# Kernel optimization log

Measured on AMD Instinct MI355X. Metric: run time of the kernel, lower is better.

## Reference

```python
import jax, jax.numpy as jnp
import numpy as np

N, K, D = 50000, 32, 128


def setup_inputs() -> dict:
    key = jax.random.key(0)
    k1, k2, k3, k4 = jax.random.split(key, 4)
    v_fea = jax.random.normal(k1, (N, D), dtype=jnp.float32)
    t_emb = jax.random.normal(k2, (N, D), dtype=jnp.float32)
    ef = jax.random.randint(k3, (N, K), 0, N, dtype=jnp.int64)
    # nn.Linear(2D, 2D, bias=False) weight, scaled like torch default init
    W = jax.random.normal(k4, (2 * D, 2 * D), dtype=jnp.float32) * (1.0 / np.sqrt(2 * D))
    return {"v_fea": v_fea, "t_emb": t_emb, "ef": ef, "W": W}


def reference(v_fea, t_emb, ef, W):
    # v: gathered neighbor features [N, K, D]
    v = v_fea[ef]
    # q: [N, 2D]; torch Linear applies x @ W.T
    q = jnp.concatenate([v_fea, t_emb], axis=-1)
    wq = q @ W.T                                   # [N, 2D]
    # k: [N, K, 2D]
    k = jnp.concatenate([v, t_emb[ef]], axis=-1)
    # per-edge score: bmm(k, wq[..., None]) -> [N, K]
    r = jnp.einsum("nkd,nd->nk", k, wq)
    r = jax.nn.softmax(r, axis=1)                  # softmax over neighbors
    # weighted sum over neighbors -> [N, D]
    ef_fea = jnp.einsum("nk,nkd->nd", r, v)
    return ef_fea
```

## Files before the change

kernel.cpp:

```cpp
#include <hip/hip_runtime.h>
#include <hip/hip_bf16.h>

#define D     128
#define TWO_D 256
#define KNB   32

typedef __attribute__((ext_vector_type(8))) short    s8;
typedef __attribute__((ext_vector_type(8))) _Float16 h8;
typedef __attribute__((ext_vector_type(4))) float    f4;

__device__ inline unsigned short f2h(float f) {
    return __builtin_bit_cast(unsigned short, (_Float16)f);
}
__device__ inline float h2f(unsigned short u) {
    return (float)__builtin_bit_cast(_Float16, u);
}

__global__ __launch_bounds__(256) void cast_kernel(
    const float* __restrict__ a, const float* __restrict__ b,
    unsigned short* __restrict__ oa, unsigned short* __restrict__ ob, int n4)
{
    int i = blockIdx.x * 256 + threadIdx.x;
    if (i >= n4) return;
    float4 x = ((const float4*)a)[i];
    float4 y = ((const float4*)b)[i];
    ushort4 px = make_ushort4(f2h(x.x), f2h(x.y), f2h(x.z), f2h(x.w));
    ushort4 py = make_ushort4(f2h(y.x), f2h(y.y), f2h(y.z), f2h(y.w));
    ((ushort4*)oa)[i] = px;
    ((ushort4*)ob)[i] = py;
}

#define BM 128
#define BN 128
#define BK 32
#define LDT 56

template<bool WQ_F32>
__global__ __launch_bounds__(256) void gemm_wq_mfma(
    const float* __restrict__ v_fea, const float* __restrict__ t_emb,
    const float* __restrict__ W, float* __restrict__ wq_f,
    unsigned short* __restrict__ wq_h, int M)
{
    __shared__ unsigned short As[BM][LDT];
    __shared__ unsigned short Bs[BN][LDT];

    const int tid  = threadIdx.x;
    const int w    = tid >> 6;
    const int lane = tid & 63;
    const int quad = lane >> 4;
    const int l16  = lane & 15;
    const int row0 = blockIdx.x * BM;
    const int i0   = blockIdx.y * BN;

    f4 acc[2][8] = {};

    const int srow = tid >> 1;
    const int skh  = (tid & 1) * 16;
    int ga = row0 + srow; if (ga >= M) ga = M - 1;

    for (int kt = 0; kt < TWO_D; kt += BK) {
        const float* srcA = (kt < D) ? v_fea : t_emb;
        const int kb = kt & (D - 1);
        const float* pa = srcA + (size_t)ga * D + kb + skh;
        const float* pb = W + (size_t)(i0 + srow) * TWO_D + kt + skh;
        float4 av0 = *(const float4*)(pa);
        float4 av1 = *(const float4*)(pa + 4);
        float4 av2 = *(const float4*)(pa + 8);
        float4 av3 = *(const float4*)(pa + 12);
        float4 bv0 = *(const float4*)(pb);
        float4 bv1 = *(const float4*)(pb + 4);
        float4 bv2 = *(const float4*)(pb + 8);
        float4 bv3 = *(const float4*)(pb + 12);

        __syncthreads();
        {
            s8 p0, p1;
            p0[0]=(short)f2h(av0.x); p0[1]=(short)f2h(av0.y); p0[2]=(short)f2h(av0.z); p0[3]=(short)f2h(av0.w);
            p0[4]=(short)f2h(av1.x); p0[5]=(short)f2h(av1.y); p0[6]=(short)f2h(av1.z); p0[7]=(short)f2h(av1.w);
            p1[0]=(short)f2h(av2.x); p1[1]=(short)f2h(av2.y); p1[2]=(short)f2h(av2.z); p1[3]=(short)f2h(av2.w);
            p1[4]=(short)f2h(av3.x); p1[5]=(short)f2h(av3.y); p1[6]=(short)f2h(av3.z); p1[7]=(short)f2h(av3.w);
            *(s8*)&As[srow][skh]     = p0;
            *(s8*)&As[srow][skh + 8] = p1;
            s8 q0, q1;
            q0[0]=(short)f2h(bv0.x); q0[1]=(short)f2h(bv0.y); q0[2]=(short)f2h(bv0.z); q0[3]=(short)f2h(bv0.w);
            q0[4]=(short)f2h(bv1.x); q0[5]=(short)f2h(bv1.y); q0[6]=(short)f2h(bv1.z); q0[7]=(short)f2h(bv1.w);
            q1[0]=(short)f2h(bv2.x); q1[1]=(short)f2h(bv2.y); q1[2]=(short)f2h(bv2.z); q1[3]=(short)f2h(bv2.w);
            q1[4]=(short)f2h(bv3.x); q1[5]=(short)f2h(bv3.y); q1[6]=(short)f2h(bv3.z); q1[7]=(short)f2h(bv3.w);
            *(s8*)&Bs[srow][skh]     = q0;
            *(s8*)&Bs[srow][skh + 8] = q1;
        }
        __syncthreads();

        s8 af0 = *(const s8*)&As[w * 32 + l16][quad * 8];
        s8 af1 = *(const s8*)&As[w * 32 + 16 + l16][quad * 8];
#pragma unroll
        for (int nt = 0; nt < 8; ++nt) {
            s8 bf = *(const s8*)&Bs[nt * 16 + l16][quad * 8];
            acc[0][nt] = __builtin_amdgcn_mfma_f32_16x16x32_f16(
                __builtin_bit_cast(h8, af0), __builtin_bit_cast(h8, bf), acc[0][nt], 0, 0, 0);
            acc[1][nt] = __builtin_amdgcn_mfma_f32_16x16x32_f16(
                __builtin_bit_cast(h8, af1), __builtin_bit_cast(h8, bf), acc[1][nt], 0, 0, 0);
        }
    }

#pragma unroll
    for (int mt = 0; mt < 2; ++mt) {
#pragma unroll
        for (int nt = 0; nt < 8; ++nt) {
#pragma unroll
            for (int r = 0; r < 4; ++r) {
                int grow = row0 + w * 32 + mt * 16 + quad * 4 + r;
                if (grow < M) {
                    int gcol = i0 + nt * 16 + l16;
                    if (WQ_F32) wq_f[(size_t)grow * TWO_D + gcol] = acc[mt][nt][r];
                    else        wq_h[(size_t)grow * TWO_D + gcol] = f2h(acc[mt][nt][r]);
                }
            }
        }
    }
}

template<bool WQ_F32>
__global__ __launch_bounds__(256) void attn_kernel(
    const unsigned short* __restrict__ vh, const unsigned short* __restrict__ th,
    const int* __restrict__ ef, const float* __restrict__ wq_f,
    const unsigned short* __restrict__ wq_h, float* __restrict__ outp, int M)
{
    __shared__ unsigned short v_cache[4][KNB][D];

    const int lane = threadIdx.x & 63;
    const int w    = threadIdx.x >> 6;
    const int n    = blockIdx.x * 4 + w;
    if (n >= M) return;

    const int l16  = lane & 15;
    const int gsel = (lane >> 4) & 1;
    const unsigned short* gsrc = (lane < 32) ? vh : th;

    float wv[8];
    if (WQ_F32) {
        const float* p = wq_f + (size_t)n * TWO_D + ((lane >> 5) << 7) + l16 * 8;
        float4 c0 = *(const float4*)p;
        float4 c1 = *(const float4*)(p + 4);
        wv[0]=c0.x; wv[1]=c0.y; wv[2]=c0.z; wv[3]=c0.w;
        wv[4]=c1.x; wv[5]=c1.y; wv[6]=c1.z; wv[7]=c1.w;
    } else {
        s8 h = *(const s8*)(wq_h + (size_t)n * TWO_D + ((lane >> 5) << 7) + l16 * 8);
#pragma unroll
        for (int j = 0; j < 8; ++j) wv[j] = h2f((unsigned short)h[j]);
    }

    int eidx = 0;
    if (lane < KNB) eidx = ef[n * KNB + lane];

    float myscore = -1e30f;
#pragma unroll
    for (int k = 0; k < KNB; k += 2) {
        int e = __shfl(eidx, k + gsel, 64);
        s8 x = *(const s8*)(gsrc + (size_t)e * D + l16 * 8);
        if (lane < 32) *(s8*)&v_cache[w][k + gsel][l16 * 8] = x;
        float p = 0.f;
#pragma unroll
        for (int j = 0; j < 8; ++j) p = fmaf(h2f((unsigned short)x[j]), wv[j], p);
#pragma unroll
        for (int off = 8; off > 0; off >>= 1) p += __shfl_xor(p, off, 64);
        p += __shfl_xor(p, 32, 64);
        float po = __shfl_xor(p, 16, 64);
        float s_even = gsel ? po : p;
        float s_odd  = gsel ? p  : po;
        if (lane == k)     myscore = s_even;
        if (lane == k + 1) myscore = s_odd;
    }

    float mx = myscore;
#pragma unroll
    for (int off = 16; off > 0; off >>= 1) mx = fmaxf(mx, __shfl_xor(mx, off, 64));
    float ex  = __expf(myscore - mx);
    float sum = ex;
#pragma unroll
    for (int off = 16; off > 0; off >>= 1) sum += __shfl_xor(sum, off, 64);
    float r = ex / sum;

    float2 o = make_float2(0.f, 0.f);
#pragma unroll
    for (int k = 0; k < KNB; ++k) {
        float rk = __shfl(r, k, 64);
        unsigned int pq = *(const unsigned int*)&v_cache[w][k][lane * 2];
        o.x = fmaf(rk, h2f((unsigned short)(pq & 0xFFFFu)), o.x);
        o.y = fmaf(rk, h2f((unsigned short)(pq >> 16)), o.y);
    }
    *(float2*)(outp + (size_t)n * D + lane * 2) = o;
}

extern "C" void kernel_launch(void* const* d_in, const int* in_sizes, int n_in,
                              void* d_out, int out_size, void* d_ws, size_t ws_size,
                              hipStream_t stream)
{
    const float* v_fea = (const float*)d_in[0];
    const float* t_emb = (const float*)d_in[1];
    const int*   ef    = (const int*)d_in[2];
    const float* W     = (const float*)d_in[3];
    float* outp = (float*)d_out;

    const int M = in_sizes[0] / D;
    const size_t gath = (size_t)M * D * 2;
    const size_t wq_f32_bytes = (size_t)M * TWO_D * 4;
    const bool wqf32 = ws_size >= wq_f32_bytes + 2 * gath;

    char* ws = (char*)d_ws;
    float*          wq_f = (float*)ws;
    unsigned short* wq_h = (unsigned short*)ws;
    const size_t wq_bytes = wqf32 ? wq_f32_bytes : (size_t)M * TWO_D * 2;
    unsigned short* vh = (unsigned short*)(ws + wq_bytes);
    unsigned short* th = (unsigned short*)(ws + wq_bytes + gath);

    const int n4 = M * D / 4;
    cast_kernel<<<(n4 + 255) / 256, 256, 0, stream>>>(v_fea, t_emb, vh, th, n4);

    dim3 gg((M + BM - 1) / BM, TWO_D / BN);
    if (wqf32) {
        gemm_wq_mfma<true><<<gg, 256, 0, stream>>>(v_fea, t_emb, W, wq_f, wq_h, M);
        attn_kernel<true><<<(M + 3) / 4, 256, 0, stream>>>(vh, th, ef, wq_f, wq_h, outp, M);
    } else {
        gemm_wq_mfma<false><<<gg, 256, 0, stream>>>(v_fea, t_emb, W, wq_f, wq_h, M);
        attn_kernel<false><<<(M + 3) / 4, 256, 0, stream>>>(vh, th, ef, wq_f, wq_h, outp, M);
    }
}
```

Before: 251.5 us.

## Use fp16 wq always, read pre-cast inputs in GEMM, batch gathers, use fdot2

The GEMM now loads the fp16 copies of v_fea/t_emb produced by the cast kernel instead of re-reading and converting fp32 inputs. wq is always stored in fp16, which halves its write and read traffic. The attention kernel issues all 16 gather loads up front to raise memory-level parallelism, and computes scores with packed fp16 dot2 instructions. The costs are more live registers (16 s8 vectors) and slightly lower score precision from the fp16 wq.

```diff
diff --git a/kernel.cpp b/kernel.cpp
--- a/kernel.cpp
+++ b/kernel.cpp
@@ -7,6 +7,7 @@
 
 typedef __attribute__((ext_vector_type(8))) short    s8;
 typedef __attribute__((ext_vector_type(8))) _Float16 h8;
+typedef __attribute__((ext_vector_type(2))) _Float16 h2v;
 typedef __attribute__((ext_vector_type(4))) float    f4;
 
 __device__ inline unsigned short f2h(float f) {
@@ -14,6 +15,22 @@
 }
 __device__ inline float h2f(unsigned short u) {
     return (float)__builtin_bit_cast(_Float16, u);
+}
+
+union v16u { s8 s; h2v h[4]; };
+
+__device__ inline float dot8(s8 x, s8 w, float acc) {
+#if __has_builtin(__builtin_amdgcn_fdot2)
+    v16u ux, uw; ux.s = x; uw.s = w;
+#pragma unroll
+    for (int j = 0; j < 4; ++j)
+        acc = __builtin_amdgcn_fdot2(ux.h[j], uw.h[j], acc, false);
+#else
+#pragma unroll
+    for (int j = 0; j < 8; ++j)
+        acc = fmaf(h2f((unsigned short)x[j]), h2f((unsigned short)w[j]), acc);
+#endif
+    return acc;
 }
 
 __global__ __launch_bounds__(256) void cast_kernel(
@@ -35,11 +52,9 @@
 #define BK 32
 #define LDT 56
 
-template<bool WQ_F32>
 __global__ __launch_bounds__(256) void gemm_wq_mfma(
-    const float* __restrict__ v_fea, const float* __restrict__ t_emb,
-    const float* __restrict__ W, float* __restrict__ wq_f,
-    unsigned short* __restrict__ wq_h, int M)
+    const unsigned short* __restrict__ vh, const unsigned short* __restrict__ th,
+    const float* __restrict__ W, unsigned short* __restrict__ wq_h, int M)
 {
     __shared__ unsigned short As[BM][LDT];
     __shared__ unsigned short Bs[BN][LDT];
@@ -55,39 +70,32 @@
     f4 acc[2][8] = {};
 
     const int srow = tid >> 1;
-    const int skh  = (tid & 1) * 16;
+    const int seg  = tid & 1;
     int ga = row0 + srow; if (ga >= M) ga = M - 1;
 
     for (int kt = 0; kt < TWO_D; kt += BK) {
-        const float* srcA = (kt < D) ? v_fea : t_emb;
+        const unsigned short* srcA = (kt < D) ? vh : th;
         const int kb = kt & (D - 1);
-        const float* pa = srcA + (size_t)ga * D + kb + skh;
-        const float* pb = W + (size_t)(i0 + srow) * TWO_D + kt + skh;
-        float4 av0 = *(const float4*)(pa);
-        float4 av1 = *(const float4*)(pa + 4);
-        float4 av2 = *(const float4*)(pa + 8);
-        float4 av3 = *(const float4*)(pa + 12);
-        float4 bv0 = *(const float4*)(pb);
-        float4 bv1 = *(const float4*)(pb + 4);
-        float4 bv2 = *(const float4*)(pb + 8);
-        float4 bv3 = *(const float4*)(pb + 12);
+        const unsigned short* pa = srcA + (size_t)ga * D + kb + seg * 16;
+        s8 a0 = *(const s8*)(pa);
+        s8 a1 = *(const s8*)(pa + 8);
+        const float* pb = W + (size_t)(i0 + srow) * TWO_D + kt + seg * 16;
+        float4 b0 = *(const float4*)(pb);
+        float4 b1 = *(const float4*)(pb + 4);
+        float4 b2 = *(const float4*)(pb + 8);
+        float4 b3 = *(const float4*)(pb + 12);
 
         __syncthreads();
+        *(s8*)&As[srow][seg * 16]     = a0;
+        *(s8*)&As[srow][seg * 16 + 8] = a1;
         {
-            s8 p0, p1;
-            p0[0]=(short)f2h(av0.x); p0[1]=(short)f2h(av0.y); p0[2]=(short)f2h(av0.z); p0[3]=(short)f2h(av0.w);
-            p0[4]=(short)f2h(av1.x); p0[5]=(short)f2h(av1.y); p0[6]=(short)f2h(av1.z); p0[7]=(short)f2h(av1.w);
-            p1[0]=(short)f2h(av2.x); p1[1]=(short)f2h(av2.y); p1[2]=(short)f2h(av2.z); p1[3]=(short)f2h(av2.w);
-            p1[4]=(short)f2h(av3.x); p1[5]=(short)f2h(av3.y); p1[6]=(short)f2h(av3.z); p1[7]=(short)f2h(av3.w);
-            *(s8*)&As[srow][skh]     = p0;
-            *(s8*)&As[srow][skh + 8] = p1;
             s8 q0, q1;
-            q0[0]=(short)f2h(bv0.x); q0[1]=(short)f2h(bv0.y); q0[2]=(short)f2h(bv0.z); q0[3]=(short)f2h(bv0.w);
-            q0[4]=(short)f2h(bv1.x); q0[5]=(short)f2h(bv1.y); q0[6]=(short)f2h(bv1.z); q0[7]=(short)f2h(bv1.w);
-            q1[0]=(short)f2h(bv2.x); q1[1]=(short)f2h(bv2.y); q1[2]=(short)f2h(bv2.z); q1[3]=(short)f2h(bv2.w);
-            q1[4]=(short)f2h(bv3.x); q1[5]=(short)f2h(bv3.y); q1[6]=(short)f2h(bv3.z); q1[7]=(short)f2h(bv3.w);
-            *(s8*)&Bs[srow][skh]     = q0;
-            *(s8*)&Bs[srow][skh + 8] = q1;
+            q0[0]=(short)f2h(b0.x); q0[1]=(short)f2h(b0.y); q0[2]=(short)f2h(b0.z); q0[3]=(short)f2h(b0.w);
+            q0[4]=(short)f2h(b1.x); q0[5]=(short)f2h(b1.y); q0[6]=(short)f2h(b1.z); q0[7]=(short)f2h(b1.w);
+            q1[0]=(short)f2h(b2.x); q1[1]=(short)f2h(b2.y); q1[2]=(short)f2h(b2.z); q1[3]=(short)f2h(b2.w);
+            q1[4]=(short)f2h(b3.x); q1[5]=(short)f2h(b3.y); q1[6]=(short)f2h(b3.z); q1[7]=(short)f2h(b3.w);
+            *(s8*)&Bs[srow][seg * 16]     = q0;
+            *(s8*)&Bs[srow][seg * 16 + 8] = q1;
         }
         __syncthreads();
 
@@ -110,21 +118,17 @@
 #pragma unroll
             for (int r = 0; r < 4; ++r) {
                 int grow = row0 + w * 32 + mt * 16 + quad * 4 + r;
-                if (grow < M) {
-                    int gcol = i0 + nt * 16 + l16;
-                    if (WQ_F32) wq_f[(size_t)grow * TWO_D + gcol] = acc[mt][nt][r];
-                    else        wq_h[(size_t)grow * TWO_D + gcol] = f2h(acc[mt][nt][r]);
-                }
+                if (grow < M)
+                    wq_h[(size_t)grow * TWO_D + i0 + nt * 16 + l16] = f2h(acc[mt][nt][r]);
             }
         }
     }
 }
 
-template<bool WQ_F32>
 __global__ __launch_bounds__(256) void attn_kernel(
     const unsigned short* __restrict__ vh, const unsigned short* __restrict__ th,
-    const int* __restrict__ ef, const float* __restrict__ wq_f,
-    const unsigned short* __restrict__ wq_h, float* __restrict__ outp, int M)
+    const int* __restrict__ ef, const unsigned short* __restrict__ wq_h,
+    float* __restrict__ outp, int M)
 {
     __shared__ unsigned short v_cache[4][KNB][D];
 
@@ -137,31 +141,24 @@
     const int gsel = (lane >> 4) & 1;
     const unsigned short* gsrc = (lane < 32) ? vh : th;
 
-    float wv[8];
-    if (WQ_F32) {
-        const float* p = wq_f + (size_t)n * TWO_D + ((lane >> 5) << 7) + l16 * 8;
-        float4 c0 = *(const float4*)p;
-        float4 c1 = *(const float4*)(p + 4);
-        wv[0]=c0.x; wv[1]=c0.y; wv[2]=c0.z; wv[3]=c0.w;
-        wv[4]=c1.x; wv[5]=c1.y; wv[6]=c1.z; wv[7]=c1.w;
-    } else {
-        s8 h = *(const s8*)(wq_h + (size_t)n * TWO_D + ((lane >> 5) << 7) + l16 * 8);
-#pragma unroll
-        for (int j = 0; j < 8; ++j) wv[j] = h2f((unsigned short)h[j]);
-    }
+    s8 wq8 = *(const s8*)(wq_h + (size_t)n * TWO_D + ((lane >> 5) << 7) + l16 * 8);
 
     int eidx = 0;
     if (lane < KNB) eidx = ef[n * KNB + lane];
 
+    s8 xs[16];
+#pragma unroll
+    for (int kk = 0; kk < 16; ++kk) {
+        int e = __shfl(eidx, 2 * kk + gsel, 64);
+        xs[kk] = *(const s8*)(gsrc + (size_t)e * D + l16 * 8);
+    }
+
     float myscore = -1e30f;
 #pragma unroll
-    for (int k = 0; k < KNB; k += 2) {
-        int e = __shfl(eidx, k + gsel, 64);
-        s8 x = *(const s8*)(gsrc + (size_t)e * D + l16 * 8);
-        if (lane < 32) *(s8*)&v_cache[w][k + gsel][l16 * 8] = x;
-        float p = 0.f;
-#pragma unroll
-        for (int j = 0; j < 8; ++j) p = fmaf(h2f((unsigned short)x[j]), wv[j], p);
+    for (int kk = 0; kk < 16; ++kk) {
+        const int k = 2 * kk;
+        if (lane < 32) *(s8*)&v_cache[w][k + gsel][l16 * 8] = xs[kk];
+        float p = dot8(xs[kk], wq8, 0.f);
 #pragma unroll
         for (int off = 8; off > 0; off >>= 1) p += __shfl_xor(p, off, 64);
         p += __shfl_xor(p, 32, 64);
@@ -203,26 +200,15 @@
     float* outp = (float*)d_out;
 
     const int M = in_sizes[0] / D;
-    const size_t gath = (size_t)M * D * 2;
-    const size_t wq_f32_bytes = (size_t)M * TWO_D * 4;
-    const bool wqf32 = ws_size >= wq_f32_bytes + 2 * gath;
-
     char* ws = (char*)d_ws;
-    float*          wq_f = (float*)ws;
     unsigned short* wq_h = (unsigned short*)ws;
-    const size_t wq_bytes = wqf32 ? wq_f32_bytes : (size_t)M * TWO_D * 2;
-    unsigned short* vh = (unsigned short*)(ws + wq_bytes);
-    unsigned short* th = (unsigned short*)(ws + wq_bytes + gath);
+    unsigned short* vh   = (unsigned short*)(ws + (size_t)M * TWO_D * 2);
+    unsigned short* th   = (unsigned short*)(ws + (size_t)M * TWO_D * 2 + (size_t)M * D * 2);
 
     const int n4 = M * D / 4;
     cast_kernel<<<(n4 + 255) / 256, 256, 0, stream>>>(v_fea, t_emb, vh, th, n4);
 
     dim3 gg((M + BM - 1) / BM, TWO_D / BN);
-    if (wqf32) {
-        gemm_wq_mfma<true><<<gg, 256, 0, stream>>>(v_fea, t_emb, W, wq_f, wq_h, M);
-        attn_kernel<true><<<(M + 3) / 4, 256, 0, stream>>>(vh, th, ef, wq_f, wq_h, outp, M);
-    } else {
-        gemm_wq_mfma<false><<<gg, 256, 0, stream>>>(v_fea, t_emb, W, wq_f, wq_h, M);
-        attn_kernel<false><<<(M + 3) / 4, 256, 0, stream>>>(vh, th, ef, wq_f, wq_h, outp, M);
-    }
-}
+    gemm_wq_mfma<<<gg, 256, 0, stream>>>(vh, th, W, wq_h, M);
+    attn_kernel<<<(M + 3) / 4, 256, 0, stream>>>(vh, th, ef, wq_h, outp, M);
+}
```

Result: faster. 232.0 us (-7.8%).
